# Kernel tuning notes

Hardware: AMD Instinct MI355X
Metric: run time of the kernel (lower is better)

The kernel has to match this reference:

```python
import jax, jax.numpy as jnp
import numpy as np

B, T, D, HD = 4, 4096, 1024, 64

def setup_inputs() -> dict:
    key = jax.random.key(0)
    k1, k2, k3, k4 = jax.random.split(key, 4)
    scale = 1.0 / np.sqrt(D)
    return {
        "x": jax.random.normal(k1, (B, T, D), dtype=jnp.float32),
        "Wq": jax.random.normal(k2, (HD, D), dtype=jnp.float32) * scale,
        "Wk": jax.random.normal(k3, (HD, D), dtype=jnp.float32) * scale,
        "Wv": jax.random.normal(k4, (HD, D), dtype=jnp.float32) * scale,
    }

def reference(x, Wq, Wk, Wv):
    # x: [B,T,D]; W*: [head_dim, D] (torch Linear weight layout)
    Q = jnp.einsum('btd,hd->bth', x, Wq)  # [B,T,HD]
    K = jnp.einsum('btd,hd->bth', x, Wk)
    V = jnp.einsum('btd,hd->bth', x, Wv)
    hd = Q.shape[-1]
    scores = jnp.einsum('bqh,bkh->bqk', Q, K) * (hd ** -0.5)  # [B,T,T]
    t = scores.shape[1]
    causal = jnp.tril(jnp.ones((t, t), dtype=bool))
    scores = jnp.where(causal, scores, -jnp.inf)
    att = jax.nn.softmax(scores, axis=-1)
    return jnp.einsum('bqk,bkh->bqh', att, V)  # [B,T,HD]
```

## Files before the change

kernel.cpp:

```cpp
#include <hip/hip_runtime.h>
#include <stdint.h>

#define B_  4
#define T_  4096
#define D_  1024
#define HD_ 64
#define BT_ 16384

typedef short bf16x8 __attribute__((ext_vector_type(8)));
typedef float f32x4  __attribute__((ext_vector_type(4)));
typedef unsigned short u16;
typedef u16 u16x4 __attribute__((ext_vector_type(4)));
typedef unsigned int u32;
typedef u32 u32x4 __attribute__((ext_vector_type(4)));

#define M0L2_  11.54156032f
#define QSCALE_ 0.18033688f

#define SLOTS_B_ 288

__device__ __forceinline__ u16 f2bf(float f) {
    union { float f; unsigned u; } v; v.f = f;
    unsigned r = (v.u + 0x7FFF + ((v.u >> 16) & 1)) >> 16;
    return (u16)r;
}
__device__ __forceinline__ float bf2f(u16 u) {
    union { unsigned u; float f; } v; v.u = ((unsigned)u) << 16;
    return v.f;
}
__device__ __forceinline__ u32 cvt_pk_bf16(float lo, float hi) {
    u32 r;
    asm("v_cvt_pk_bf16_f32 %0, %1, %2" : "=v"(r) : "v"(lo), "v"(hi));
    return r;
}

__device__ __forceinline__ int slot_base(int qt) {
    int a = qt >> 3, r = qt & 7;
    return qt + 4 * a * (a - 1) + a * r;
}

__global__ __launch_bounds__(256) void wconv_kernel(
    const float* __restrict__ wq, const float* __restrict__ wk,
    const float* __restrict__ wv, u16* __restrict__ wb)
{
    const int j   = blockIdx.x >> 5;
    const int off = (blockIdx.x & 31) * 2048 + threadIdx.x * 8;
    const float* src = (j == 0) ? wq : ((j == 1) ? wk : wv);
    f32x4 a0 = *(const f32x4*)(src + off);
    f32x4 a1 = *(const f32x4*)(src + off + 4);
    u32x4 b;
    b[0] = cvt_pk_bf16(a0[0], a0[1]);
    b[1] = cvt_pk_bf16(a0[2], a0[3]);
    b[2] = cvt_pk_bf16(a1[0], a1[1]);
    b[3] = cvt_pk_bf16(a1[2], a1[3]);
    *(u32x4*)(wb + j * 65536 + off) = b;
}

__global__ __launch_bounds__(256) void qkv_kernel(
    const float* __restrict__ x, const u16* __restrict__ wb,
    u16* __restrict__ qs, u16* __restrict__ kss, u16* __restrict__ vssT)
{
    __shared__ __align__(16) u16 xt[32][72];
    __shared__ __align__(16) u16 wt[192][72];

    const int tid  = threadIdx.x;
    const int lane = tid & 63;
    const int w    = tid >> 6;
    const int quad = lane >> 4;
    const int l16  = lane & 15;
    const int row0 = blockIdx.x * 32;
    const int sp   = w >> 1;
    const int gh   = (w & 1) * 6;

    const int xrow = tid >> 3;
    const int xcg  = tid & 7;

    f32x4 acc[6];
    #pragma unroll
    for (int g = 0; g < 6; ++g) acc[g] = (f32x4)0.0f;

    f32x4 xa, xb;
    bf16x8 wr[6];
    {
        const float* xp = x + (size_t)(row0 + xrow) * D_ + xcg * 8;
        xa = *(const f32x4*)xp; xb = *(const f32x4*)(xp + 4);
        #pragma unroll
        for (int i = 0; i < 6; ++i) {
            int chunk = tid + 256 * i;
            wr[i] = *(const bf16x8*)(wb + (size_t)(chunk >> 3) * D_ + (chunk & 7) * 8);
        }
    }

    for (int kc = 0; kc < 16; ++kc) {
        __syncthreads();
        {
            u32x4 px;
            px[0] = cvt_pk_bf16(xa[0], xa[1]);
            px[1] = cvt_pk_bf16(xa[2], xa[3]);
            px[2] = cvt_pk_bf16(xb[0], xb[1]);
            px[3] = cvt_pk_bf16(xb[2], xb[3]);
            *(u32x4*)&xt[xrow][xcg * 8] = px;
            #pragma unroll
            for (int i = 0; i < 6; ++i) {
                int chunk = tid + 256 * i;
                *(bf16x8*)&wt[chunk >> 3][(chunk & 7) * 8] = wr[i];
            }
        }
        __syncthreads();
        if (kc < 15) {
            const float* xp = x + (size_t)(row0 + xrow) * D_ + (kc + 1) * 64 + xcg * 8;
            xa = *(const f32x4*)xp; xb = *(const f32x4*)(xp + 4);
            #pragma unroll
            for (int i = 0; i < 6; ++i) {
                int chunk = tid + 256 * i;
                wr[i] = *(const bf16x8*)(wb + (size_t)(chunk >> 3) * D_ + (kc + 1) * 64 + (chunk & 7) * 8);
            }
        }
        #pragma unroll
        for (int ks = 0; ks < 2; ++ks) {
            bf16x8 a = *(const bf16x8*)&xt[sp * 16 + l16][ks * 32 + quad * 8];
            #pragma unroll
            for (int g = 0; g < 6; ++g) {
                bf16x8 b = *(const bf16x8*)&wt[(gh + g) * 16 + l16][ks * 32 + quad * 8];
                acc[g] = __builtin_amdgcn_mfma_f32_16x16x32_bf16(a, b, acc[g], 0, 0, 0);
            }
        }
    }
    #pragma unroll
    for (int g = 0; g < 6; ++g) {
        const int n = (gh + g) * 16 + l16;
        const int j = n >> 6, h = n & 63;
        const int rbase = row0 + sp * 16 + quad * 4;
        if (j == 0) {
            #pragma unroll
            for (int r = 0; r < 4; ++r) qs[(size_t)(rbase + r) * HD_ + h] = f2bf(acc[g][r] * QSCALE_);
        } else if (j == 1) {
            #pragma unroll
            for (int r = 0; r < 4; ++r) kss[(size_t)(rbase + r) * HD_ + h] = f2bf(acc[g][r]);
        } else {
            u16x4 v;
            #pragma unroll
            for (int r = 0; r < 4; ++r) v[r] = f2bf(acc[g][r]);
            *(u16x4*)(vssT + (size_t)h * BT_ + rbase) = v;
        }
    }
}

__global__ __launch_bounds__(512, 6) void attn_kernel(
    const u16* __restrict__ qs, const u16* __restrict__ kss,
    const u16* __restrict__ vssT,
    float* __restrict__ pl, u16* __restrict__ pO)
{
    __shared__ __align__(16) u16 kt[64][72];
    __shared__ __align__(16) u16 vt[80][72];
    __shared__ __align__(16) u16 pt[8][16][72];

    const int bi  = blockIdx.x;
    const int c   = bi & 7;
    const int qt2 = (bi >> 3) & 31;
    const int b   = bi >> 8;
    const int qthi = qt2 * 2 + 1;
    if ((c << 3) > qthi) return;

    const int kt0  = c << 3;
    const int kend = ((kt0 + 7) < qthi) ? (kt0 + 7) : qthi;

    const int tid  = threadIdx.x;
    const int lane = tid & 63;
    const int w    = tid >> 6;
    const int quad = lane >> 4;
    const int l16  = lane & 15;
    const int qtw  = qt2 * 2 + (w >> 2);
    const int wr   = (w & 3) * 16;
    const size_t base = (size_t)b * T_;

    for (int idx = tid; idx < 16 * 72; idx += 512) {
        int rr = idx / 72, cc = idx - rr * 72;
        vt[64 + rr][cc] = (rr == 0) ? (u16)0x3F80 : (u16)0;
    }

    bf16x8 qf[2];
    {
        const u16* qp = qs + (base + qtw * 64 + wr + l16) * HD_ + quad * 8;
        qf[0] = *(const bf16x8*)(qp);
        qf[1] = *(const bf16x8*)(qp + 32);
    }

    f32x4 o_acc[5];
    #pragma unroll
    for (int g = 0; g < 5; ++g) o_acc[g] = (f32x4)0.0f;

    const int  lr  = (tid & 255) >> 2;
    const int  lp  = tid & 3;
    const bool isV = tid >= 256;

    const u16* sp = isV ? (vssT + (size_t)lr * BT_ + base + kt0 * 64 + lp * 16)
                        : (kss + (base + kt0 * 64 + lr) * HD_ + lp * 16);
    const ptrdiff_t step = isV ? 64 : 64 * HD_;
    u16* dst = isV ? &vt[lr][lp * 16] : &kt[lr][lp * 16];

    bf16x8 r0 = *(const bf16x8*)(sp);
    bf16x8 r1 = *(const bf16x8*)(sp + 8);
    sp += step;

    for (int kti = kt0; kti <= kend; ++kti) {
        __syncthreads();
        *(bf16x8*)(dst)     = r0;
        *(bf16x8*)(dst + 8) = r1;
        __syncthreads();
        if (kti < kend) {
            r0 = *(const bf16x8*)(sp);
            r1 = *(const bf16x8*)(sp + 8);
            sp += step;
        }

        if (kti <= qtw) {
            f32x4 s[4];
            __builtin_amdgcn_s_setprio(1);
            #pragma unroll
            for (int g = 0; g < 4; ++g) {
                s[g] = (f32x4)0.0f;
                #pragma unroll
                for (int ks = 0; ks < 2; ++ks) {
                    bf16x8 kf = *(const bf16x8*)&kt[g * 16 + l16][ks * 32 + quad * 8];
                    s[g] = __builtin_amdgcn_mfma_f32_16x16x32_bf16(qf[ks], kf, s[g], 0, 0, 0);
                }
            }
            __builtin_amdgcn_s_setprio(0);

            if (kti == qtw) {
                #pragma unroll
                for (int g = 0; g < 4; ++g) {
                    int key = kti * 64 + g * 16 + l16;
                    #pragma unroll
                    for (int r = 0; r < 4; ++r) {
                        int q = qtw * 64 + wr + quad * 4 + r;
                        if (key > q) s[g][r] = -1e30f;
                    }
                }
            }
            #pragma unroll
            for (int g = 0; g < 4; ++g) {
                #pragma unroll
                for (int r = 0; r < 4; r += 2) {
                    float e0 = __builtin_amdgcn_exp2f(s[g][r]     - M0L2_);
                    float e1 = __builtin_amdgcn_exp2f(s[g][r + 1] - M0L2_);
                    u32 pk = cvt_pk_bf16(e0, e1);
                    pt[w][quad * 4 + r][g * 16 + l16]     = (u16)pk;
                    pt[w][quad * 4 + r + 1][g * 16 + l16] = (u16)(pk >> 16);
                }
            }
            #pragma unroll
            for (int ks = 0; ks < 2; ++ks) {
                bf16x8 pa = *(const bf16x8*)&pt[w][l16][ks * 32 + quad * 8];
                __builtin_amdgcn_s_setprio(1);
                #pragma unroll
                for (int g = 0; g < 5; ++g) {
                    bf16x8 vf = *(const bf16x8*)&vt[g * 16 + l16][ks * 32 + quad * 8];
                    o_acc[g] = __builtin_amdgcn_mfma_f32_16x16x32_bf16(pa, vf, o_acc[g], 0, 0, 0);
                }
                __builtin_amdgcn_s_setprio(0);
            }
        }
    }

    const int slot = b * SLOTS_B_ + slot_base(qtw) + c;
    if (l16 == 0) {
        #pragma unroll
        for (int r = 0; r < 4; ++r)
            pl[slot * 64 + wr + quad * 4 + r] = o_acc[4][r];
    }
    #pragma unroll
    for (int g = 0; g < 4; ++g) {
        #pragma unroll
        for (int r = 0; r < 4; ++r) {
            int row = wr + quad * 4 + r;
            pO[(size_t)slot * 4096 + row * 64 + g * 16 + l16] = f2bf(o_acc[g][r]);
        }
    }
}

__global__ __launch_bounds__(256) void merge_kernel(
    const float* __restrict__ pl, const u16* __restrict__ pO,
    float* __restrict__ out)
{
    const int bi = blockIdx.x;
    const int rh = bi & 1;
    const int qt = (bi >> 1) & 63;
    const int b  = bi >> 7;
    const int nc = (qt >> 3) + 1;
    const int s0 = b * SLOTS_B_ + slot_base(qt);
    const int row = rh * 32 + (threadIdx.x >> 3);
    const int hg  = (threadIdx.x & 7) * 8;

    float L = 0.0f;
    for (int c2 = 0; c2 < nc; ++c2) L += pl[(s0 + c2) * 64 + row];

    float o[8];
    #pragma unroll
    for (int i = 0; i < 8; ++i) o[i] = 0.0f;
    for (int c2 = 0; c2 < nc; ++c2) {
        const u16* p = pO + (size_t)(s0 + c2) * 4096 + row * 64 + hg;
        bf16x8 v0 = *(const bf16x8*)p;
        #pragma unroll
        for (int i = 0; i < 8; ++i) o[i] += bf2f((u16)v0[i]);
    }
    const float inv = 1.0f / L;
    float* op = out + ((size_t)b * T_ + qt * 64 + row) * HD_ + hg;
    f32x4 v;
    #pragma unroll
    for (int i = 0; i < 4; ++i) v[i] = o[i] * inv;
    *(f32x4*)op = v;
    #pragma unroll
    for (int i = 0; i < 4; ++i) v[i] = o[4 + i] * inv;
    *(f32x4*)(op + 4) = v;
}

extern "C" void kernel_launch(void* const* d_in, const int* in_sizes, int n_in,
                              void* d_out, int out_size, void* d_ws, size_t ws_size,
                              hipStream_t stream) {
    const float* x  = (const float*)d_in[0];
    const float* wq = (const float*)d_in[1];
    const float* wk = (const float*)d_in[2];
    const float* wv = (const float*)d_in[3];

    const size_t NE = (size_t)BT_ * HD_;
    char* ws = (char*)d_ws;
    u16* qs   = (u16*)ws;
    u16* kss  = qs  + NE;
    u16* vssT = kss + NE;
    u16* wb   = vssT + NE;
    float* pl = (float*)(wb + 192 * 1024);
    u16* pO   = (u16*)(pl + 4 * SLOTS_B_ * 64);
    float* out = (float*)d_out;

    wconv_kernel<<<dim3(96),   dim3(256), 0, stream>>>(wq, wk, wv, wb);
    qkv_kernel  <<<dim3(512),  dim3(256), 0, stream>>>(x, wb, qs, kss, vssT);
    attn_kernel <<<dim3(1024), dim3(512), 0, stream>>>(qs, kss, vssT, pl, pO);
    merge_kernel<<<dim3(512),  dim3(256), 0, stream>>>(pl, pO, out);
}
```

Before: 155.9 us.

## Rework causal attention with 32x32 MFMA, paired query tiles and fixed 4-step chunks

New measurement: 146.8 us. -5.9%, faster.

```diff
diff --git a/kernel.cpp b/kernel.cpp
--- a/kernel.cpp
+++ b/kernel.cpp
@@ -9,6 +9,7 @@
 
 typedef short bf16x8 __attribute__((ext_vector_type(8)));
 typedef float f32x4  __attribute__((ext_vector_type(4)));
+typedef float f32x16 __attribute__((ext_vector_type(16)));
 typedef unsigned short u16;
 typedef u16 u16x4 __attribute__((ext_vector_type(4)));
 typedef unsigned int u32;
@@ -17,7 +18,8 @@
 #define M0L2_  11.54156032f
 #define QSCALE_ 0.18033688f
 
-#define SLOTS_B_ 288
+#define CPB_   264
+#define NSLOT_ (4 * CPB_ * 2)
 
 __device__ __forceinline__ u16 f2bf(float f) {
     union { float f; unsigned u; } v; v.f = f;
@@ -32,11 +34,6 @@
     u32 r;
     asm("v_cvt_pk_bf16_f32 %0, %1, %2" : "=v"(r) : "v"(lo), "v"(hi));
     return r;
-}
-
-__device__ __forceinline__ int slot_base(int qt) {
-    int a = qt >> 3, r = qt & 7;
-    return qt + 4 * a * (a - 1) + a * r;
 }
 
 __global__ __launch_bounds__(256) void wconv_kernel(
@@ -146,174 +143,191 @@
     }
 }
 
-__global__ __launch_bounds__(512, 6) void attn_kernel(
+__global__ __launch_bounds__(256, 4) void attn_kernel(
     const u16* __restrict__ qs, const u16* __restrict__ kss,
     const u16* __restrict__ vssT,
     float* __restrict__ pl, u16* __restrict__ pO)
 {
-    __shared__ __align__(16) u16 kt[64][72];
-    __shared__ __align__(16) u16 vt[80][72];
-    __shared__ __align__(16) u16 pt[8][16][72];
-
-    const int bi  = blockIdx.x;
-    const int c   = bi & 7;
-    const int qt2 = (bi >> 3) & 31;
-    const int b   = bi >> 8;
-    const int qthi = qt2 * 2 + 1;
-    if ((c << 3) > qthi) return;
-
-    const int kt0  = c << 3;
-    const int kend = ((kt0 + 7) < qthi) ? (kt0 + 7) : qthi;
+    __shared__ __align__(16) u16 kt2[8 * 65 * 8];
+    __shared__ __align__(16) u16 vt2[8 * 65 * 8];
+
+    const int m = blockIdx.x % CPB_;
+    const int b = blockIdx.x / CPB_;
+
+    int t0, bound, qtA, qtB;
+    if (m < 240)      { int u = m >> 4; t0 = (m & 15) * 4; bound = 2 * u + 2; qtA = u;  qtB = 30 - u; }
+    else if (m < 248) { t0 = (m - 240) * 4; bound = 1 << 30; qtA = 15; qtB = 15; }
+    else              { t0 = (m - 248) * 4; bound = 1 << 30; qtA = 31; qtB = 31; }
 
     const int tid  = threadIdx.x;
     const int lane = tid & 63;
     const int w    = tid >> 6;
-    const int quad = lane >> 4;
-    const int l16  = lane & 15;
-    const int qtw  = qt2 * 2 + (w >> 2);
-    const int wr   = (w & 3) * 16;
+    const int l31  = lane & 31;
+    const int hi   = lane >> 5;
     const size_t base = (size_t)b * T_;
 
-    for (int idx = tid; idx < 16 * 72; idx += 512) {
-        int rr = idx / 72, cc = idx - rr * 72;
-        vt[64 + rr][cc] = (rr == 0) ? (u16)0x3F80 : (u16)0;
-    }
-
-    bf16x8 qf[2];
+    int qt    = (t0 < bound) ? qtA : qtB;
+    int kti   = (t0 < bound) ? t0 : (t0 - bound);
+    int qrow0 = qt * 128 + w * 32;
+
+    bf16x8 qf[4];
+    #pragma unroll
+    for (int ds = 0; ds < 4; ++ds)
+        qf[ds] = *(const bf16x8*)(qs + (base + qrow0 + l31) * HD_ + ds * 16 + hi * 8);
+
+    f32x16 o0 = (f32x16)0.0f, o1 = (f32x16)0.0f;
+    float l_acc = 0.0f;
+
+    const int srow = tid >> 2, q4 = tid & 3;
+    const u16* kp = kss  + (base + srow) * HD_ + q4 * 16;
+    const u16* vp = vssT + (size_t)srow * BT_ + base + q4 * 16;
+    u16* kdst = kt2 + ((((srow >> 5) * 4 + q4) * 65 + (srow & 31)) * 8);
+    u16* vdst = vt2 + ((((srow >> 5) * 4 + q4) * 65 + (srow & 31)) * 8);
+
+    bf16x8 kr0, kr1, vr0, vr1;
     {
-        const u16* qp = qs + (base + qtw * 64 + wr + l16) * HD_ + quad * 8;
-        qf[0] = *(const bf16x8*)(qp);
-        qf[1] = *(const bf16x8*)(qp + 32);
-    }
-
-    f32x4 o_acc[5];
-    #pragma unroll
-    for (int g = 0; g < 5; ++g) o_acc[g] = (f32x4)0.0f;
-
-    const int  lr  = (tid & 255) >> 2;
-    const int  lp  = tid & 3;
-    const bool isV = tid >= 256;
-
-    const u16* sp = isV ? (vssT + (size_t)lr * BT_ + base + kt0 * 64 + lp * 16)
-                        : (kss + (base + kt0 * 64 + lr) * HD_ + lp * 16);
-    const ptrdiff_t step = isV ? 64 : 64 * HD_;
-    u16* dst = isV ? &vt[lr][lp * 16] : &kt[lr][lp * 16];
-
-    bf16x8 r0 = *(const bf16x8*)(sp);
-    bf16x8 r1 = *(const bf16x8*)(sp + 8);
-    sp += step;
-
-    for (int kti = kt0; kti <= kend; ++kti) {
+        const u16* k0 = kp + (size_t)kti * 64 * HD_;
+        kr0 = *(const bf16x8*)k0; kr1 = *(const bf16x8*)(k0 + 8);
+        const u16* v0 = vp + kti * 64;
+        vr0 = *(const bf16x8*)v0; vr1 = *(const bf16x8*)(v0 + 8);
+    }
+
+    auto FLUSH = [&](int role) {
+        const int slot = (b * CPB_ + m) * 2 + role;
+        u32 la = __builtin_bit_cast(u32, l_acc), lb = la;
+        asm("v_permlane32_swap_b32 %0, %1" : "+v"(la), "+v"(lb));
+        float lfull = __builtin_bit_cast(float, la) + __builtin_bit_cast(float, lb);
+        if (hi == 0) pl[slot * 128 + w * 32 + l31] = lfull;
+        #pragma unroll
+        for (int reg = 0; reg < 16; ++reg) {
+            int row = w * 32 + (reg & 3) + 8 * (reg >> 2) + 4 * hi;
+            pO[(size_t)slot * 8192 + row * 64 + l31]      = f2bf(o0[reg]);
+            pO[(size_t)slot * 8192 + row * 64 + 32 + l31] = f2bf(o1[reg]);
+        }
+    };
+
+    for (int step = 0; step < 4; ++step) {
+        const int i = t0 + step;
         __syncthreads();
-        *(bf16x8*)(dst)     = r0;
-        *(bf16x8*)(dst + 8) = r1;
+        *(bf16x8*)(kdst)       = kr0;
+        *(bf16x8*)(kdst + 256) = kr1;
+        *(bf16x8*)(vdst)       = vr0;
+        *(bf16x8*)(vdst + 256) = vr1;
         __syncthreads();
-        if (kti < kend) {
-            r0 = *(const bf16x8*)(sp);
-            r1 = *(const bf16x8*)(sp + 8);
-            sp += step;
-        }
-
-        if (kti <= qtw) {
-            f32x4 s[4];
-            __builtin_amdgcn_s_setprio(1);
-            #pragma unroll
-            for (int g = 0; g < 4; ++g) {
-                s[g] = (f32x4)0.0f;
-                #pragma unroll
-                for (int ks = 0; ks < 2; ++ks) {
-                    bf16x8 kf = *(const bf16x8*)&kt[g * 16 + l16][ks * 32 + quad * 8];
-                    s[g] = __builtin_amdgcn_mfma_f32_16x16x32_bf16(qf[ks], kf, s[g], 0, 0, 0);
-                }
-            }
-            __builtin_amdgcn_s_setprio(0);
-
-            if (kti == qtw) {
-                #pragma unroll
-                for (int g = 0; g < 4; ++g) {
-                    int key = kti * 64 + g * 16 + l16;
-                    #pragma unroll
-                    for (int r = 0; r < 4; ++r) {
-                        int q = qtw * 64 + wr + quad * 4 + r;
-                        if (key > q) s[g][r] = -1e30f;
-                    }
-                }
-            }
-            #pragma unroll
-            for (int g = 0; g < 4; ++g) {
-                #pragma unroll
-                for (int r = 0; r < 4; r += 2) {
-                    float e0 = __builtin_amdgcn_exp2f(s[g][r]     - M0L2_);
-                    float e1 = __builtin_amdgcn_exp2f(s[g][r + 1] - M0L2_);
-                    u32 pk = cvt_pk_bf16(e0, e1);
-                    pt[w][quad * 4 + r][g * 16 + l16]     = (u16)pk;
-                    pt[w][quad * 4 + r + 1][g * 16 + l16] = (u16)(pk >> 16);
-                }
-            }
-            #pragma unroll
-            for (int ks = 0; ks < 2; ++ks) {
-                bf16x8 pa = *(const bf16x8*)&pt[w][l16][ks * 32 + quad * 8];
+
+        int kti_next = 0;
+        if (step < 3) {
+            kti_next = (i + 1 < bound) ? (i + 1) : (i + 1 - bound);
+            const u16* k0 = kp + (size_t)kti_next * 64 * HD_;
+            kr0 = *(const bf16x8*)k0; kr1 = *(const bf16x8*)(k0 + 8);
+            const u16* v0 = vp + kti_next * 64;
+            vr0 = *(const bf16x8*)v0; vr1 = *(const bf16x8*)(v0 + 8);
+        }
+
+        if (kti * 64 <= qrow0 + 31) {
+            const bool diag = (kti * 64 + 63 > qrow0);
+            const int  qa   = qrow0 + l31;
+            u32 wv[16];
+            #pragma unroll
+            for (int kg = 0; kg < 2; ++kg) {
+                f32x16 s = (f32x16)0.0f;
                 __builtin_amdgcn_s_setprio(1);
                 #pragma unroll
-                for (int g = 0; g < 5; ++g) {
-                    bf16x8 vf = *(const bf16x8*)&vt[g * 16 + l16][ks * 32 + quad * 8];
-                    o_acc[g] = __builtin_amdgcn_mfma_f32_16x16x32_bf16(pa, vf, o_acc[g], 0, 0, 0);
+                for (int ds = 0; ds < 4; ++ds) {
+                    bf16x8 af = *(const bf16x8*)(kt2 + ((kg * 4 + ds) * 65 + lane) * 8);
+                    s = __builtin_amdgcn_mfma_f32_32x32x16_bf16(af, qf[ds], s, 0, 0, 0);
                 }
                 __builtin_amdgcn_s_setprio(0);
-            }
-        }
-    }
-
-    const int slot = b * SLOTS_B_ + slot_base(qtw) + c;
-    if (l16 == 0) {
-        #pragma unroll
-        for (int r = 0; r < 4; ++r)
-            pl[slot * 64 + wr + quad * 4 + r] = o_acc[4][r];
-    }
-    #pragma unroll
-    for (int g = 0; g < 4; ++g) {
-        #pragma unroll
-        for (int r = 0; r < 4; ++r) {
-            int row = wr + quad * 4 + r;
-            pO[(size_t)slot * 4096 + row * 64 + g * 16 + l16] = f2bf(o_acc[g][r]);
-        }
-    }
+                float lp = 0.0f;
+                #pragma unroll
+                for (int rp = 0; rp < 8; ++rp) {
+                    float e0 = __builtin_amdgcn_exp2f(s[2 * rp]     - M0L2_);
+                    float e1 = __builtin_amdgcn_exp2f(s[2 * rp + 1] - M0L2_);
+                    if (diag) {
+                        const int k0e = kti * 64 + kg * 32 + ((2 * rp) & 3) + 8 * ((2 * rp) >> 2) + 4 * hi;
+                        if (k0e > qa)     e0 = 0.0f;
+                        if (k0e + 1 > qa) e1 = 0.0f;
+                    }
+                    lp += e0 + e1;
+                    wv[kg * 8 + rp] = cvt_pk_bf16(e0, e1);
+                }
+                l_acc += lp;
+            }
+            bf16x8 pa[4];
+            #pragma unroll
+            for (int ks = 0; ks < 4; ++ks) {
+                const int kg2 = ks >> 1, k1 = ks & 1;
+                u32 x0 = wv[kg2 * 8 + k1 * 4 + 0], y0 = wv[kg2 * 8 + k1 * 4 + 2];
+                u32 x1 = wv[kg2 * 8 + k1 * 4 + 1], y1 = wv[kg2 * 8 + k1 * 4 + 3];
+                asm("v_permlane32_swap_b32 %0, %1" : "+v"(x0), "+v"(y0));
+                asm("v_permlane32_swap_b32 %0, %1" : "+v"(x1), "+v"(y1));
+                u32x4 t; t[0] = x0; t[1] = x1; t[2] = y0; t[3] = y1;
+                pa[ks] = __builtin_bit_cast(bf16x8, t);
+            }
+            __builtin_amdgcn_s_setprio(1);
+            #pragma unroll
+            for (int ks = 0; ks < 4; ++ks) {
+                bf16x8 vf0 = *(const bf16x8*)(vt2 + ((0 * 4 + ks) * 65 + lane) * 8);
+                o0 = __builtin_amdgcn_mfma_f32_32x32x16_bf16(pa[ks], vf0, o0, 0, 0, 0);
+                bf16x8 vf1 = *(const bf16x8*)(vt2 + ((1 * 4 + ks) * 65 + lane) * 8);
+                o1 = __builtin_amdgcn_mfma_f32_32x32x16_bf16(pa[ks], vf1, o1, 0, 0, 0);
+            }
+            __builtin_amdgcn_s_setprio(0);
+        }
+
+        kti = kti_next;
+        if (step < 3 && (i + 1) == bound) {
+            FLUSH(0);
+            o0 = (f32x16)0.0f; o1 = (f32x16)0.0f; l_acc = 0.0f;
+            qt = qtB; qrow0 = qt * 128 + w * 32;
+            #pragma unroll
+            for (int ds = 0; ds < 4; ++ds)
+                qf[ds] = *(const bf16x8*)(qs + (base + qrow0 + l31) * HD_ + ds * 16 + hi * 8);
+        }
+    }
+    FLUSH((t0 + 3 >= bound) ? 1 : 0);
 }
 
 __global__ __launch_bounds__(256) void merge_kernel(
     const float* __restrict__ pl, const u16* __restrict__ pO,
     float* __restrict__ out)
 {
-    const int bi = blockIdx.x;
-    const int rh = bi & 1;
-    const int qt = (bi >> 1) & 63;
-    const int b  = bi >> 7;
-    const int nc = (qt >> 3) + 1;
-    const int s0 = b * SLOTS_B_ + slot_base(qt);
-    const int row = rh * 32 + (threadIdx.x >> 3);
-    const int hg  = (threadIdx.x & 7) * 8;
+    const int bi  = blockIdx.x;
+    const int rh  = bi & 1;
+    const int qt2 = (bi >> 1) & 31;
+    const int b   = bi >> 6;
+
+    int c0, c1, role, mbase;
+    if (qt2 <= 14)      { int u = qt2;      c0 = 0;                 c1 = (2 * u + 1) >> 2; role = 0; mbase = u * 16; }
+    else if (qt2 == 15) { c0 = 0;           c1 = 7;                 role = 0; mbase = 240; }
+    else if (qt2 <= 30) { int u = 30 - qt2; c0 = (2 * u + 2) >> 2;  c1 = 15; role = 1; mbase = u * 16; }
+    else                { c0 = 0;           c1 = 15;                role = 0; mbase = 248; }
+
+    const int row = rh * 64 + (threadIdx.x >> 2);
+    const int hg  = (threadIdx.x & 3) * 16;
 
     float L = 0.0f;
-    for (int c2 = 0; c2 < nc; ++c2) L += pl[(s0 + c2) * 64 + row];
-
-    float o[8];
-    #pragma unroll
-    for (int i = 0; i < 8; ++i) o[i] = 0.0f;
-    for (int c2 = 0; c2 < nc; ++c2) {
-        const u16* p = pO + (size_t)(s0 + c2) * 4096 + row * 64 + hg;
+    float o[16];
+    #pragma unroll
+    for (int i = 0; i < 16; ++i) o[i] = 0.0f;
+    for (int c = c0; c <= c1; ++c) {
+        const int slot = (b * CPB_ + mbase + c) * 2 + role;
+        L += pl[slot * 128 + row];
+        const u16* p = pO + (size_t)slot * 8192 + row * 64 + hg;
         bf16x8 v0 = *(const bf16x8*)p;
-        #pragma unroll
-        for (int i = 0; i < 8; ++i) o[i] += bf2f((u16)v0[i]);
+        bf16x8 v1 = *(const bf16x8*)(p + 8);
+        #pragma unroll
+        for (int i = 0; i < 8; ++i) { o[i] += bf2f((u16)v0[i]); o[8 + i] += bf2f((u16)v1[i]); }
     }
     const float inv = 1.0f / L;
-    float* op = out + ((size_t)b * T_ + qt * 64 + row) * HD_ + hg;
-    f32x4 v;
-    #pragma unroll
-    for (int i = 0; i < 4; ++i) v[i] = o[i] * inv;
-    *(f32x4*)op = v;
-    #pragma unroll
-    for (int i = 0; i < 4; ++i) v[i] = o[4 + i] * inv;
-    *(f32x4*)(op + 4) = v;
+    float* op = out + ((size_t)b * T_ + qt2 * 128 + row) * HD_ + hg;
+    #pragma unroll
+    for (int j = 0; j < 4; ++j) {
+        f32x4 v;
+        #pragma unroll
+        for (int i = 0; i < 4; ++i) v[i] = o[j * 4 + i] * inv;
+        *(f32x4*)(op + j * 4) = v;
+    }
 }
 
 extern "C" void kernel_launch(void* const* d_in, const int* in_sizes, int n_in,
@@ -331,11 +345,11 @@
     u16* vssT = kss + NE;
     u16* wb   = vssT + NE;
     float* pl = (float*)(wb + 192 * 1024);
-    u16* pO   = (u16*)(pl + 4 * SLOTS_B_ * 64);
+    u16* pO   = (u16*)(pl + (size_t)NSLOT_ * 128);
     float* out = (float*)d_out;
 
-    wconv_kernel<<<dim3(96),   dim3(256), 0, stream>>>(wq, wk, wv, wb);
-    qkv_kernel  <<<dim3(512),  dim3(256), 0, stream>>>(x, wb, qs, kss, vssT);
-    attn_kernel <<<dim3(1024), dim3(512), 0, stream>>>(qs, kss, vssT, pl, pO);
-    merge_kernel<<<dim3(512),  dim3(256), 0, stream>>>(pl, pO, out);
-}
+    wconv_kernel<<<dim3(96),        dim3(256), 0, stream>>>(wq, wk, wv, wb);
+    qkv_kernel  <<<dim3(512),       dim3(256), 0, stream>>>(x, wb, qs, kss, vssT);
+    attn_kernel <<<dim3(4 * CPB_),  dim3(256), 0, stream>>>(qs, kss, vssT, pl, pO);
+    merge_kernel<<<dim3(256),       dim3(256), 0, stream>>>(pl, pO, out);
+}
```
